# Kernel tuning notes

Hardware: AMD Instinct MI355X
Metric: run time of the kernel (lower is better)

## Reference

```python
import jax, jax.numpy as jnp
import numpy as np

B, T, N, D, M, H, L, FF = 8, 128, 24, 128, 9, 8, 4, 1024
F = D // H          # spatial head dim = 16
HD = D // H         # temporal head dim = 16
ND = N * D          # 3072
NM = N * M          # 216


def setup_inputs() -> dict:
    key = jax.random.key(0)
    ks = jax.random.split(key, 24)
    w = lambda k, shape, s=0.05: (jax.random.normal(k, shape, jnp.float32) * s)
    z = lambda shape: jnp.zeros(shape, jnp.float32)
    return {
        "inputs": jax.random.normal(ks[0], (B, T, NM), jnp.float32),
        "emb_W": w(ks[1], (N, M, D)), "emb_b": z((N, D)),
        "sp_Wq": w(ks[2], (L, H, N, D, F)), "sp_bq": z((L, H, N, F)),
        "sp_Wk": w(ks[3], (L, H, D, F)), "sp_bk": z((L, H, F)),
        "sp_Wv": w(ks[4], (L, H, D, F)), "sp_bv": z((L, H, F)),
        "tmp_Win": w(ks[5], (L, N, 3 * D, D)), "tmp_bin": z((L, N, 3 * D)),
        "tmp_Wout": w(ks[6], (L, N, D, D)), "tmp_bout": z((L, N, D)),
        "ff_W1": w(ks[7], (L, ND, FF)), "ff_b1": z((L, FF)),
        "ff_W2": w(ks[8], (L, FF, ND)), "ff_b2": z((L, ND)),
        "ln_g": jnp.ones((L, ND), jnp.float32), "ln_b": z((L, ND)),
        "fin_W": w(ks[9], (ND, NM)), "fin_b": z((NM,)),
    }


def _ln(x, g, b):
    m = jnp.mean(x, -1, keepdims=True)
    v = jnp.mean(jnp.square(x - m), -1, keepdims=True)
    return (x - m) * jax.lax.rsqrt(v + 1e-5) * g + b


def _pos_encoding():
    # standard sinusoidal PE; original adds it over the FIRST axis of the
    # (B, T, N*D) tensor (applied before the permute), so index by B.
    pos = jnp.arange(B, dtype=jnp.float32)[:, None]
    div = jnp.exp(jnp.arange(0, ND, 2, dtype=jnp.float32) * (-np.log(10000.0) / ND))
    pe = jnp.zeros((B, ND), jnp.float32)
    pe = pe.at[:, 0::2].set(jnp.sin(pos * div)).at[:, 1::2].set(jnp.cos(pos * div))
    return pe


def reference(inputs, emb_W, emb_b, sp_Wq, sp_bq, sp_Wk, sp_bk, sp_Wv, sp_bv,
              tmp_Win, tmp_bin, tmp_Wout, tmp_bout, ff_W1, ff_b1, ff_W2, ff_b2,
              ln_g, ln_b, fin_W, fin_b):
    # joint embedding: (B,T,N,M) @ (N,M,D) -> (B,T,N,D)
    x4 = inputs.reshape(B, T, N, M)
    emb = (jnp.einsum('btnm,nmd->btnd', x4, emb_W) + emb_b).reshape(B, T, ND)
    emb = emb + _pos_encoding()[:, None, :]
    h = emb.transpose(1, 0, 2)                     # (T, B, ND)
    # PyTorch float attn_mask is ADDED to scores: +1.0 strictly below diagonal
    mask = jnp.tril(jnp.ones((T, T), jnp.float32), -1)
    for l in range(L):
        xr = h.reshape(T, B, N, D)
        # ---- spatial attention (shared K/V, per-joint Q, per head) ----
        k = jnp.einsum('tbnd,hdf->tbhnf', xr, sp_Wk[l]) + sp_bk[l][:, None, :]
        v = jnp.einsum('tbnd,hdf->tbhnf', xr, sp_Wv[l]) + sp_bv[l][:, None, :]
        q = jnp.einsum('tbnd,hndf->tbhnf', xr, sp_Wq[l]) + sp_bq[l]
        a = jax.nn.softmax(jnp.einsum('tbhnf,tbhmf->tbhnm', q, k) / jnp.sqrt(jnp.float32(F)), -1)
        sp = jnp.einsum('tbhnm,tbhmf->tbhnf', a, v)
        sp = sp.transpose(0, 1, 3, 2, 4).reshape(T, B, ND)   # joint-major, heads concat within joint
        sp = _ln(sp + h, ln_g[l], ln_b[l])
        # ---- temporal attention (per-joint nn.MultiheadAttention) ----
        Wq_t, Wk_t, Wv_t = tmp_Win[l, :, :D], tmp_Win[l, :, D:2 * D], tmp_Win[l, :, 2 * D:]
        bq_t, bk_t, bv_t = tmp_bin[l, :, :D], tmp_bin[l, :, D:2 * D], tmp_bin[l, :, 2 * D:]
        qt = (jnp.einsum('tbnd,ned->tbne', xr, Wq_t) + bq_t).reshape(T, B, N, H, HD)
        kt = (jnp.einsum('tbnd,ned->tbne', xr, Wk_t) + bk_t).reshape(T, B, N, H, HD)
        vt = (jnp.einsum('tbnd,ned->tbne', xr, Wv_t) + bv_t).reshape(T, B, N, H, HD)
        st = jnp.einsum('tbnhe,sbnhe->bnhts', qt, kt) / jnp.sqrt(jnp.float32(HD)) + mask
        at = jax.nn.softmax(st, -1)
        ot = jnp.einsum('bnhts,sbnhe->tbnhe', at, vt).reshape(T, B, N, D)
        tp = (jnp.einsum('tbnd,nod->tbno', ot, tmp_Wout[l]) + tmp_bout[l]).reshape(T, B, ND)
        tp = _ln(tp + h, ln_g[l], ln_b[l])
        # ---- FFN (no activation in original) + residual + shared LN ----
        a2 = sp + tp
        o = (a2 @ ff_W1[l] + ff_b1[l]) @ ff_W2[l] + ff_b2[l]
        h = _ln(o + a2, ln_g[l], ln_b[l])
    out = h @ fin_W + fin_b                        # (T, B, NM)
    return out.transpose(1, 0, 2) + inputs
```

## Files before the change

### kernel.cpp

```cpp
#include <hip/hip_runtime.h>
#include <hip/hip_bf16.h>
#include <math.h>

constexpr int kB = 8, kT = 128, kN = 24, kD = 128, kM = 9, kH = 8, kL = 4, kFF = 1024;
constexpr int kF = 16;
constexpr int kHD = 16;
constexpr int kND = kN * kD;
constexpr int kNM = kN * kM;
constexpr int kP = kB * kT;

using bf16x8 = __attribute__((ext_vector_type(8))) short;
using f32x4  = __attribute__((ext_vector_type(4))) float;
typedef __hip_bfloat16 bf16;

__device__ __forceinline__ void load_lds16(const void* g, void* l) {
  __builtin_amdgcn_global_load_lds(
      (const __attribute__((address_space(1))) void*)g,
      (__attribute__((address_space(3))) void*)l, 16, 0, 0);
}

template<int BM, int BN, bool OUTBF>
__global__ __launch_bounds__(256) void mfma_gemm(
    const bf16* __restrict__ A, const bf16* __restrict__ Bm,
    const float* __restrict__ bias, void* __restrict__ Cv,
    int M, int Nc, int K, int ldB, int sAi, int sCi,
    long offAg, long offBg, long offCg, int sBg)
{
  constexpr int WM = BM / 2, WN = BN / 2;
  constexpr int MT = WM / 16, NT = WN / 16;
  constexpr int ASLOTS = BM * 4;
  constexpr int BSLOTS = BN * 4;
  __shared__ __align__(16) bf16 As[BM * 32];
  __shared__ __align__(16) bf16 Bs[BN * 32];

  int g = blockIdx.z;
  A  += offAg * g;
  Bm += offBg * g;
  long cbase = offCg * (long)g;
  int bOff = sBg * g;

  int m0 = blockIdx.y * BM, n0 = blockIdx.x * BN;
  int tid = threadIdx.x, lane = tid & 63, wave = tid >> 6;
  int wm = wave >> 1, wn = wave & 1;
  int fr = lane & 15, fq = lane >> 4;

  f32x4 acc[MT][NT] = {};

  for (int kk = 0; kk < K; kk += 32) {
#pragma unroll
    for (int s = tid; s < ASLOTS; s += 256) {
      int m = s >> 2, k8 = (s & 3) * 8;
      load_lds16(A + (size_t)(m0 + m) * sAi + (kk + k8), &As[s * 8]);
    }
#pragma unroll
    for (int s = tid; s < BSLOTS; s += 256) {
      int n = s >> 2, k8 = (s & 3) * 8;
      int nr = n0 + n; if (nr > Nc - 1) nr = Nc - 1;
      load_lds16(Bm + (size_t)nr * ldB + (kk + k8), &Bs[s * 8]);
    }
    __syncthreads();
    bf16x8 af[MT], bf[NT];
#pragma unroll
    for (int i = 0; i < MT; i++)
      af[i] = *(const bf16x8*)&As[(wm * WM + i * 16 + fr) * 32 + fq * 8];
#pragma unroll
    for (int j = 0; j < NT; j++)
      bf[j] = *(const bf16x8*)&Bs[(wn * WN + j * 16 + fr) * 32 + fq * 8];
#pragma unroll
    for (int i = 0; i < MT; i++)
#pragma unroll
      for (int j = 0; j < NT; j++)
        acc[i][j] = __builtin_amdgcn_mfma_f32_16x16x32_bf16(af[i], bf[j], acc[i][j], 0, 0, 0);
    __syncthreads();
  }

#pragma unroll
  for (int i = 0; i < MT; i++) {
    int row = m0 + wm * WM + i * 16 + fq * 4;
#pragma unroll
    for (int j = 0; j < NT; j++) {
      int col = n0 + wn * WN + j * 16 + fr;
      if (col < Nc) {
        float bv = bias ? bias[bOff + col] : 0.f;
#pragma unroll
        for (int r = 0; r < 4; r++) {
          long ci = cbase + (size_t)(row + r) * sCi + col;
          float v = acc[i][j][r] + bv;
          if (OUTBF) ((bf16*)Cv)[ci] = __float2bfloat16(v);
          else       ((float*)Cv)[ci] = v;
        }
      }
    }
  }
}


__global__ __launch_bounds__(256) void trans_cvt_kernel(
    const float* __restrict__ in, bf16* __restrict__ out,
    int R, int C, long inStrideZ, long outStrideZ)
{
  __shared__ float t[64][65];
  int c0 = blockIdx.x * 64, r0 = blockIdx.y * 64;
  in  += inStrideZ  * blockIdx.z;
  out += outStrideZ * blockIdx.z;
  int tx = threadIdx.x & 63, ty = threadIdx.x >> 6;
  for (int rr = ty; rr < 64; rr += 4) {
    int r = r0 + rr, c = c0 + tx;
    t[rr][tx] = (r < R && c < C) ? in[(size_t)r * C + c] : 0.f;
  }
  __syncthreads();
  for (int cc = ty; cc < 64; cc += 4) {
    int c = c0 + cc, r = r0 + tx;
    if (c < C && r < R) out[(size_t)c * R + r] = __float2bfloat16(t[tx][cc]);
  }
}

__global__ __launch_bounds__(256) void cvt_kernel(
    const float* __restrict__ in, bf16* __restrict__ out, int n)
{
  int i = blockIdx.x * 256 + threadIdx.x;
  if (i < n) out[i] = __float2bfloat16(in[i]);
}

__global__ __launch_bounds__(256) void build_spW_kernel(
    const float* __restrict__ Wq, const float* __restrict__ Wk,
    const float* __restrict__ Wv, const float* __restrict__ Win,
    bf16* __restrict__ outW)
{
  int i = blockIdx.x * 256 + threadIdx.x;
  int d = i & 127;
  int rest = i >> 7;
  int r = rest % 768;
  int n = (rest / 768) % 24;
  int l = rest / (768 * 24);
  int hh = (r & 127) >> 4, f = r & 15;
  float v;
  if (r < 128)      v = Wq[((((size_t)l * kH + hh) * kN + n) * kD + d) * kF + f];
  else if (r < 256) v = Wk[(((size_t)l * kH + hh) * kD + d) * kF + f];
  else if (r < 384) v = Wv[(((size_t)l * kH + hh) * kD + d) * kF + f];
  else              v = Win[(((size_t)l * kN + n) * 384 + (r - 384)) * kD + d];
  outW[i] = __float2bfloat16(v);
}

__global__ __launch_bounds__(256) void build_spb_kernel(
    const float* __restrict__ bq, const float* __restrict__ bk,
    const float* __restrict__ bv, const float* __restrict__ bin,
    float* __restrict__ outb)
{
  int i = blockIdx.x * 256 + threadIdx.x;
  if (i >= kL * 24 * 768) return;
  int r = i % 768;
  int n = (i / 768) % 24;
  int l = i / (768 * 24);
  int hh = (r & 127) >> 4, f = r & 15;
  float v;
  if (r < 128)      v = bq[(((size_t)l * kH + hh) * kN + n) * kF + f];
  else if (r < 256) v = bk[((size_t)l * kH + hh) * kF + f];
  else if (r < 384) v = bv[((size_t)l * kH + hh) * kF + f];
  else              v = bin[((size_t)l * kN + n) * 384 + (r - 384)];
  outb[i] = v;
}

__global__ __launch_bounds__(256) void emb_kernel(
    const float* __restrict__ inp, const float* __restrict__ W,
    const float* __restrict__ bias, float* __restrict__ h, bf16* __restrict__ hbb)
{
  int p = blockIdx.x;
  int t = p / kB, b = p % kB;
  __shared__ float xs[kNM];
  for (int i = threadIdx.x; i < kNM; i += 256)
    xs[i] = inp[((size_t)b * kT + t) * kNM + i];
  __syncthreads();
  const float c1 = -logf(10000.f) / (float)kND;
  for (int c = threadIdx.x; c < kND; c += 256) {
    int n = c / kD, d = c % kD;
    float acc = bias[n * kD + d];
#pragma unroll
    for (int m = 0; m < kM; m++)
      acc += xs[n * kM + m] * W[(n * kM + m) * kD + d];
    float ang = (float)b * expf((float)(c & ~1) * c1);
    acc += (c & 1) ? cosf(ang) : sinf(ang);
    h[(size_t)p * kND + c] = acc;
    hbb[(size_t)p * kND + c] = __float2bfloat16(acc);
  }
}

__global__ __launch_bounds__(192) void sp_attn_kernel(
    const bf16* __restrict__ qkv, float* __restrict__ out)
{
  int p = blockIdx.x;
  __shared__ float s[24 * 385];
  for (int i = threadIdx.x; i < 24 * 384; i += 192) {
    int n = i / 384, c = i % 384;
    s[n * 385 + c] = __bfloat162float(qkv[((size_t)n * kP + p) * 768 + c]);
  }
  __syncthreads();
  int hh = threadIdx.x / 24, n = threadIdx.x % 24;
  const float* qr = s + n * 385 + hh * 16;
  float sc[24];
  float mx = -1e30f;
#pragma unroll
  for (int m = 0; m < 24; m++) {
    const float* kr = s + m * 385 + 128 + hh * 16;
    float d = 0.f;
#pragma unroll
    for (int f = 0; f < 16; f++) d += qr[f] * kr[f];
    d *= 0.25f;
    sc[m] = d;
    mx = fmaxf(mx, d);
  }
  float sum = 0.f;
#pragma unroll
  for (int m = 0; m < 24; m++) { float e = __expf(sc[m] - mx); sc[m] = e; sum += e; }
  float inv = 1.f / sum;
  float* orow = out + (size_t)p * kND + n * kD + hh * 16;
#pragma unroll
  for (int f = 0; f < 16; f++) {
    float acc = 0.f;
#pragma unroll
    for (int m = 0; m < 24; m++) acc += sc[m] * s[m * 385 + 256 + hh * 16 + f];
    orow[f] = acc * inv;
  }
}

__global__ __launch_bounds__(128) void t_attn_mfma(
    const bf16* __restrict__ qkv, bf16* __restrict__ ot)
{
  int g = blockIdx.x;
  int hh = g & 7, n = (g >> 3) % 24, b = g / 192;
  __shared__ __align__(16) ushort Qs[128][32];
  __shared__ __align__(16) ushort Ks[128][32];
  __shared__ __align__(16) ushort Vt[16][136];
  __shared__ __align__(16) ushort Ps[128][136];

  for (int idx = threadIdx.x; idx < 1024; idx += 128) {
    int t = idx >> 3, e2 = (idx & 7) * 2;
    const ushort* src = (const ushort*)qkv +
        ((size_t)n * kP + (size_t)t * kB + b) * 768 + 384 + hh * 16 + e2;
    ushort2 q2 = *(const ushort2*)(src);
    ushort2 k2 = *(const ushort2*)(src + 128);
    ushort2 v2 = *(const ushort2*)(src + 256);
    *(ushort2*)&Qs[t][e2] = q2;
    *(ushort2*)&Ks[t][e2] = k2;
    *(ushort2*)&Qs[t][16 + e2] = make_ushort2(0, 0);
    *(ushort2*)&Ks[t][16 + e2] = make_ushort2(0, 0);
    Vt[e2][t] = v2.x;
    Vt[e2 + 1][t] = v2.y;
  }
  __syncthreads();

  int lane = threadIdx.x & 63, w = threadIdx.x >> 6;
  int c = lane & 15, quad = lane >> 4;

  bf16x8 aq[4];
#pragma unroll
  for (int mt = 0; mt < 4; mt++)
    aq[mt] = *(const bf16x8*)&Qs[w * 64 + mt * 16 + c][quad * 8];
  f32x4 acc[4][8];
#pragma unroll
  for (int nt = 0; nt < 8; nt++) {
    bf16x8 bk = *(const bf16x8*)&Ks[nt * 16 + c][quad * 8];
#pragma unroll
    for (int mt = 0; mt < 4; mt++) {
      f32x4 z = {0.f, 0.f, 0.f, 0.f};
      acc[mt][nt] = __builtin_amdgcn_mfma_f32_16x16x32_bf16(aq[mt], bk, z, 0, 0, 0);
    }
  }

  f32x4 invv[4];
#pragma unroll
  for (int mt = 0; mt < 4; mt++) {
    int tbase = w * 64 + mt * 16 + quad * 4;
    f32x4 rm = {-1e30f, -1e30f, -1e30f, -1e30f};
#pragma unroll
    for (int nt = 0; nt < 8; nt++) {
      int s = nt * 16 + c;
#pragma unroll
      for (int r = 0; r < 4; r++) {
        float x = acc[mt][nt][r] * 0.25f + ((s < tbase + r) ? 1.f : 0.f);
        acc[mt][nt][r] = x;
        rm[r] = fmaxf(rm[r], x);
      }
    }
#pragma unroll
    for (int off = 1; off < 16; off <<= 1)
#pragma unroll
      for (int r = 0; r < 4; r++) rm[r] = fmaxf(rm[r], __shfl_xor(rm[r], off, 64));
    f32x4 rs = {0.f, 0.f, 0.f, 0.f};
#pragma unroll
    for (int nt = 0; nt < 8; nt++)
#pragma unroll
      for (int r = 0; r < 4; r++) {
        float pp = __expf(acc[mt][nt][r] - rm[r]);
        acc[mt][nt][r] = pp;
        rs[r] += pp;
      }
#pragma unroll
    for (int off = 1; off < 16; off <<= 1)
#pragma unroll
      for (int r = 0; r < 4; r++) rs[r] += __shfl_xor(rs[r], off, 64);
#pragma unroll
    for (int r = 0; r < 4; r++) invv[mt][r] = 1.f / rs[r];
#pragma unroll
    for (int nt = 0; nt < 8; nt++)
#pragma unroll
      for (int r = 0; r < 4; r++) {
        bf16 pb = __float2bfloat16(acc[mt][nt][r]);
        Ps[tbase + r][nt * 16 + c] = *(ushort*)&pb;
      }
  }

  f32x4 o[4] = {};
#pragma unroll
  for (int ks = 0; ks < 128; ks += 32) {
    bf16x8 bv = *(const bf16x8*)&Vt[c][ks + quad * 8];
#pragma unroll
    for (int mt = 0; mt < 4; mt++) {
      bf16x8 ap = *(const bf16x8*)&Ps[w * 64 + mt * 16 + c][ks + quad * 8];
      o[mt] = __builtin_amdgcn_mfma_f32_16x16x32_bf16(ap, bv, o[mt], 0, 0, 0);
    }
  }

#pragma unroll
  for (int mt = 0; mt < 4; mt++) {
#pragma unroll
    for (int r = 0; r < 4; r++) {
      int t = w * 64 + mt * 16 + quad * 4 + r;
      float val = o[mt][r] * invv[mt][r];
      ot[((size_t)n * kP + (size_t)t * kB + b) * 128 + hh * 16 + c] = __float2bfloat16(val);
    }
  }
}

__global__ __launch_bounds__(256) void fuse_a2_kernel(
    const float* __restrict__ sp, const float* __restrict__ tp,
    const float* __restrict__ h, const float* __restrict__ g,
    const float* __restrict__ be, float* __restrict__ a2, bf16* __restrict__ a2b)
{
  int row = blockIdx.x;
  const float* s1p = sp + (size_t)row * kND;
  const float* s2p = tp + (size_t)row * kND;
  const float* hp  = h  + (size_t)row * kND;
  float x1[12], x2[12];
  float sum1 = 0.f, sum2 = 0.f;
#pragma unroll
  for (int i = 0; i < 12; i++) {
    int c = threadIdx.x + 256 * i;
    float hv = hp[c];
    x1[i] = s1p[c] + hv; x2[i] = s2p[c] + hv;
    sum1 += x1[i]; sum2 += x2[i];
  }
  __shared__ float red1[4], red2[4];
#pragma unroll
  for (int o = 32; o > 0; o >>= 1) { sum1 += __shfl_down(sum1, o, 64); sum2 += __shfl_down(sum2, o, 64); }
  int wid = threadIdx.x >> 6;
  if ((threadIdx.x & 63) == 0) { red1[wid] = sum1; red2[wid] = sum2; }
  __syncthreads();
  float mean1 = (red1[0] + red1[1] + red1[2] + red1[3]) * (1.f / kND);
  float mean2 = (red2[0] + red2[1] + red2[2] + red2[3]) * (1.f / kND);
  __syncthreads();
  float v1 = 0.f, v2 = 0.f;
#pragma unroll
  for (int i = 0; i < 12; i++) {
    float d1 = x1[i] - mean1, d2 = x2[i] - mean2;
    v1 += d1 * d1; v2 += d2 * d2;
  }
#pragma unroll
  for (int o = 32; o > 0; o >>= 1) { v1 += __shfl_down(v1, o, 64); v2 += __shfl_down(v2, o, 64); }
  if ((threadIdx.x & 63) == 0) { red1[wid] = v1; red2[wid] = v2; }
  __syncthreads();
  float r1 = rsqrtf((red1[0] + red1[1] + red1[2] + red1[3]) * (1.f / kND) + 1e-5f);
  float r2 = rsqrtf((red2[0] + red2[1] + red2[2] + red2[3]) * (1.f / kND) + 1e-5f);
#pragma unroll
  for (int i = 0; i < 12; i++) {
    int c = threadIdx.x + 256 * i;
    float gc = g[c], bc = be[c];
    float o = (x1[i] - mean1) * r1 * gc + bc + (x2[i] - mean2) * r2 * gc + bc;
    a2[(size_t)row * kND + c] = o;
    a2b[(size_t)row * kND + c] = __float2bfloat16(o);
  }
}

__global__ __launch_bounds__(256) void add_ln_dual_kernel(
    const float* __restrict__ a, const float* __restrict__ b,
    const float* __restrict__ g, const float* __restrict__ be,
    float* __restrict__ out, bf16* __restrict__ outb)
{
  int row = blockIdx.x;
  const float* ar = a + (size_t)row * kND;
  const float* br = b + (size_t)row * kND;
  float v[12];
  float s = 0.f;
#pragma unroll
  for (int i = 0; i < 12; i++) {
    int c = threadIdx.x + 256 * i;
    float x = ar[c] + br[c];
    v[i] = x; s += x;
  }
  __shared__ float red[4];
#pragma unroll
  for (int o = 32; o > 0; o >>= 1) s += __shfl_down(s, o, 64);
  int wid = threadIdx.x >> 6;
  if ((threadIdx.x & 63) == 0) red[wid] = s;
  __syncthreads();
  float mean = (red[0] + red[1] + red[2] + red[3]) * (1.f / kND);
  __syncthreads();
  float vs = 0.f;
#pragma unroll
  for (int i = 0; i < 12; i++) { float d = v[i] - mean; vs += d * d; }
#pragma unroll
  for (int o = 32; o > 0; o >>= 1) vs += __shfl_down(vs, o, 64);
  if ((threadIdx.x & 63) == 0) red[wid] = vs;
  __syncthreads();
  float rstd = rsqrtf((red[0] + red[1] + red[2] + red[3]) * (1.f / kND) + 1e-5f);
#pragma unroll
  for (int i = 0; i < 12; i++) {
    int c = threadIdx.x + 256 * i;
    float o = (v[i] - mean) * rstd * g[c] + be[c];
    out[(size_t)row * kND + c] = o;
    outb[(size_t)row * kND + c] = __float2bfloat16(o);
  }
}

__global__ __launch_bounds__(256) void ff1_reduce_kernel(
    const float* __restrict__ part, const float* __restrict__ bias,
    bf16* __restrict__ out)
{
  int i4 = (blockIdx.x * 256 + threadIdx.x) * 4;
  const size_t S = (size_t)kP * kFF;
  float4 p0 = *(const float4*)(part + i4);
  float4 p1 = *(const float4*)(part + S + i4);
  float4 p2 = *(const float4*)(part + 2 * S + i4);
  int col = i4 & (kFF - 1);
#pragma unroll
  for (int j = 0; j < 4; j++) {
    float v = ((const float*)&p0)[j] + ((const float*)&p1)[j] + ((const float*)&p2)[j]
            + bias[col + j];
    out[i4 + j] = __float2bfloat16(v);
  }
}

__global__ __launch_bounds__(256) void final_reduce_add_kernel(
    const float* __restrict__ part, const float* __restrict__ fin_b,
    const float* __restrict__ inp, float* __restrict__ out)
{
  int i = blockIdx.x * 256 + threadIdx.x;
  if (i >= kB * kT * kNM) return;
  int c = i % kNM;
  int rem = i / kNM;
  int t = rem % kT, b = rem / kT;
  size_t pi = (size_t)(t * kB + b) * kNM + c;
  const size_t S = (size_t)kP * kNM;
  float v = fin_b[c] + inp[i];
#pragma unroll
  for (int z = 0; z < 8; z++) v += part[z * S + pi];
  out[i] = v;
}

extern "C" void kernel_launch(void* const* d_in, const int* in_sizes, int n_in,
                              void* d_out, int out_size, void* d_ws, size_t ws_size,
                              hipStream_t stream)
{
  const float* inputs   = (const float*)d_in[0];
  const float* emb_W    = (const float*)d_in[1];
  const float* emb_b    = (const float*)d_in[2];
  const float* sp_Wq    = (const float*)d_in[3];
  const float* sp_bq    = (const float*)d_in[4];
  const float* sp_Wk    = (const float*)d_in[5];
  const float* sp_bk    = (const float*)d_in[6];
  const float* sp_Wv    = (const float*)d_in[7];
  const float* sp_bv    = (const float*)d_in[8];
  const float* tmp_Win  = (const float*)d_in[9];
  const float* tmp_bin  = (const float*)d_in[10];
  const float* tmp_Wout = (const float*)d_in[11];
  const float* tmp_bout = (const float*)d_in[12];
  const float* ff_W1    = (const float*)d_in[13];
  const float* ff_b1    = (const float*)d_in[14];
  const float* ff_W2    = (const float*)d_in[15];
  const float* ff_b2    = (const float*)d_in[16];
  const float* ln_g     = (const float*)d_in[17];
  const float* ln_b     = (const float*)d_in[18];
  const float* fin_W    = (const float*)d_in[19];
  const float* fin_b    = (const float*)d_in[20];
  float* out = (float*)d_out;

  char* wp = (char*)d_ws;
  size_t off = 0;
  auto alloc = [&](size_t bytes) { void* p = wp + off; off += (bytes + 255) & ~(size_t)255; return p; };
  bf16* spW   = (bf16*)alloc((size_t)kL * 24 * 768 * 128 * 2);
  bf16* toWb  = (bf16*)alloc((size_t)kL * 24 * 128 * 128 * 2);
  bf16* W1t   = (bf16*)alloc((size_t)kL * kFF * kND * 2);
  bf16* W2t   = (bf16*)alloc((size_t)kL * kND * kFF * 2);
  bf16* finWt = (bf16*)alloc((size_t)kNM * kND * 2);
  float* spbc = (float*)alloc((size_t)kL * 24 * 768 * 4);
  float* hb   = (float*)alloc((size_t)kP * kND * 4);
  bf16*  hbb  = (bf16*) alloc((size_t)kP * kND * 2);
  bf16*  qkvb = (bf16*) alloc((size_t)24 * kP * 768 * 2);
  float* sp   = (float*)alloc((size_t)kP * kND * 4);
  float* tp   = (float*)alloc((size_t)kP * kND * 4);
  float* a2   = (float*)alloc((size_t)kP * kND * 4);
  bf16*  a2b  = (bf16*) alloc((size_t)kP * kND * 2);
  bf16*  f1b  = (bf16*) alloc((size_t)kP * kFF * 2);
  bf16*  otb  = (bf16*) alloc((size_t)24 * kP * 128 * 2);
  float* ffpart  = sp;
  float* finpart = tp;

  trans_cvt_kernel<<<dim3(kFF / 64, kND / 64, kL), 256, 0, stream>>>(
      ff_W1, W1t, kND, kFF, (long)kND * kFF, (long)kFF * kND);
  trans_cvt_kernel<<<dim3(kND / 64, kFF / 64, kL), 256, 0, stream>>>(
      ff_W2, W2t, kFF, kND, (long)kFF * kND, (long)kND * kFF);
  trans_cvt_kernel<<<dim3((kNM + 63) / 64, kND / 64, 1), 256, 0, stream>>>(
      fin_W, finWt, kND, kNM, 0L, 0L);
  cvt_kernel<<<(kL * 24 * 128 * 128 + 255) / 256, 256, 0, stream>>>(
      tmp_Wout, toWb, kL * 24 * 128 * 128);
  build_spW_kernel<<<(kL * 24 * 768 * 128) / 256, 256, 0, stream>>>(
      sp_Wq, sp_Wk, sp_Wv, tmp_Win, spW);
  build_spb_kernel<<<(kL * 24 * 768 + 255) / 256, 256, 0, stream>>>(
      sp_bq, sp_bk, sp_bv, tmp_bin, spbc);

  emb_kernel<<<kP, 256, 0, stream>>>(inputs, emb_W, emb_b, hb, hbb);

  for (int l = 0; l < kL; l++) {
    const float* lg = ln_g + (size_t)l * kND;
    const float* lb = ln_b + (size_t)l * kND;

    mfma_gemm<128, 128, true><<<dim3(6, 8, 24), 256, 0, stream>>>(
        hbb, spW + (size_t)l * 24 * 768 * 128, spbc + (size_t)l * 24 * 768, qkvb,
        kP, 768, 128, 128, kND, 768,
        128, 768 * 128, (long)kP * 768, 768);

    sp_attn_kernel<<<kP, 192, 0, stream>>>(qkvb, sp);
    t_attn_mfma<<<kB * 24 * 8, 128, 0, stream>>>(qkvb, otb);

    mfma_gemm<64, 64, false><<<dim3(2, 16, 24), 256, 0, stream>>>(
        otb, toWb + (size_t)l * 24 * 128 * 128, tmp_bout + (size_t)l * 24 * 128, tp,
        kP, 128, 128, 128, 128, kND,
        (long)kP * 128, 128 * 128, 128, 128);

    fuse_a2_kernel<<<kP, 256, 0, stream>>>(sp, tp, hb, lg, lb, a2, a2b);

    mfma_gemm<64, 64, false><<<dim3(kFF / 64, kP / 64, 3), 256, 0, stream>>>(
        a2b, W1t + (size_t)l * kFF * kND, nullptr, ffpart,
        kP, kFF, kND / 3, kND, kND, kFF,
        kND / 3, kND / 3, (long)kP * kFF, 0);
    ff1_reduce_kernel<<<(kP * kFF / 4) / 256, 256, 0, stream>>>(
        ffpart, ff_b1 + (size_t)l * kFF, f1b);

    mfma_gemm<64, 64, false><<<dim3(kND / 64, kP / 64, 1), 256, 0, stream>>>(
        f1b, W2t + (size_t)l * kND * kFF, ff_b2 + (size_t)l * kND, tp,
        kP, kND, kFF, kFF, kFF, kND, 0, 0, 0, 0);

    add_ln_dual_kernel<<<kP, 256, 0, stream>>>(tp, a2, lg, lb, hb, hbb);
  }

  mfma_gemm<64, 64, false><<<dim3((kNM + 63) / 64, kP / 64, 8), 256, 0, stream>>>(
      hbb, finWt, nullptr, finpart,
      kP, kNM, kND / 8, kND, kND, kNM,
      kND / 8, kND / 8, (long)kP * kNM, 0);
  final_reduce_add_kernel<<<(kB * kT * kNM + 255) / 256, 256, 0, stream>>>(
      finpart, fin_b, inputs, out);
}
```

Baseline: 903.0 us.

## Deepen GEMM K-tile to 64, stage epilogue through LDS, widen attention loads

The MFMA GEMM now loads 64-wide K slices per iteration, which halves the number of barrier pairs per K sweep. Its epilogue stages accumulators through shared memory so each thread writes 16 contiguous outputs with vector stores instead of scattered scalar stores. The spatial and temporal attention kernels load qkv with 4-element vector reads instead of scalar or 2-element reads, and the spatial LDS row stride is padded for float4 alignment. The trade-offs are doubled LDS per block, extra barriers in the epilogue, and an assumption that N is a multiple of 16 columns per chunk.

```diff
diff --git a/kernel.cpp b/kernel.cpp
--- a/kernel.cpp
+++ b/kernel.cpp
@@ -28,10 +28,13 @@
 {
   constexpr int WM = BM / 2, WN = BN / 2;
   constexpr int MT = WM / 16, NT = WN / 16;
-  constexpr int ASLOTS = BM * 4;
-  constexpr int BSLOTS = BN * 4;
-  __shared__ __align__(16) bf16 As[BM * 32];
-  __shared__ __align__(16) bf16 Bs[BN * 32];
+  constexpr int ASLOTS = BM * 8;
+  constexpr int BSLOTS = BN * 8;
+  constexpr int CSTR = BN + 4;
+  __shared__ __align__(16) char smem[(BM + BN) * 64 * 2];
+  bf16* As = (bf16*)smem;
+  bf16* Bs = (bf16*)(smem + BM * 64 * 2);
+  float* Cs = (float*)smem;
 
   int g = blockIdx.z;
   A  += offAg * g;
@@ -46,49 +49,80 @@
 
   f32x4 acc[MT][NT] = {};
 
-  for (int kk = 0; kk < K; kk += 32) {
+  for (int kk = 0; kk < K; kk += 64) {
 #pragma unroll
     for (int s = tid; s < ASLOTS; s += 256) {
-      int m = s >> 2, k8 = (s & 3) * 8;
+      int m = s >> 3, k8 = (s & 7) * 8;
       load_lds16(A + (size_t)(m0 + m) * sAi + (kk + k8), &As[s * 8]);
     }
 #pragma unroll
     for (int s = tid; s < BSLOTS; s += 256) {
-      int n = s >> 2, k8 = (s & 3) * 8;
+      int n = s >> 3, k8 = (s & 7) * 8;
       int nr = n0 + n; if (nr > Nc - 1) nr = Nc - 1;
       load_lds16(Bm + (size_t)nr * ldB + (kk + k8), &Bs[s * 8]);
     }
     __syncthreads();
-    bf16x8 af[MT], bf[NT];
-#pragma unroll
-    for (int i = 0; i < MT; i++)
-      af[i] = *(const bf16x8*)&As[(wm * WM + i * 16 + fr) * 32 + fq * 8];
+#pragma unroll
+    for (int ks = 0; ks < 2; ks++) {
+      bf16x8 af[MT], bfr[NT];
+#pragma unroll
+      for (int i = 0; i < MT; i++)
+        af[i] = *(const bf16x8*)&As[(wm * WM + i * 16 + fr) * 64 + ks * 32 + fq * 8];
+#pragma unroll
+      for (int j = 0; j < NT; j++)
+        bfr[j] = *(const bf16x8*)&Bs[(wn * WN + j * 16 + fr) * 64 + ks * 32 + fq * 8];
+#pragma unroll
+      for (int i = 0; i < MT; i++)
+#pragma unroll
+        for (int j = 0; j < NT; j++)
+          acc[i][j] = __builtin_amdgcn_mfma_f32_16x16x32_bf16(af[i], bfr[j], acc[i][j], 0, 0, 0);
+    }
+    __syncthreads();
+  }
+
+  constexpr int NCHUNK = BN / 16;
+  int tcol = tid & (NCHUNK - 1);
+  int trow = tid / NCHUNK;
+  int colbase = n0 + tcol * 16;
+  float vb[16];
+  if (trow < 32) {
+#pragma unroll
+    for (int jj = 0; jj < 16; jj++)
+      vb[jj] = bias ? bias[bOff + colbase + jj] : 0.f;
+  }
+#pragma unroll
+  for (int i = 0; i < MT; i++) {
+    __syncthreads();
 #pragma unroll
     for (int j = 0; j < NT; j++)
-      bf[j] = *(const bf16x8*)&Bs[(wn * WN + j * 16 + fr) * 32 + fq * 8];
-#pragma unroll
-    for (int i = 0; i < MT; i++)
-#pragma unroll
-      for (int j = 0; j < NT; j++)
-        acc[i][j] = __builtin_amdgcn_mfma_f32_16x16x32_bf16(af[i], bf[j], acc[i][j], 0, 0, 0);
+#pragma unroll
+      for (int r = 0; r < 4; r++)
+        Cs[(wm * 16 + fq * 4 + r) * CSTR + wn * WN + j * 16 + fr] = acc[i][j][r];
     __syncthreads();
-  }
-
-#pragma unroll
-  for (int i = 0; i < MT; i++) {
-    int row = m0 + wm * WM + i * 16 + fq * 4;
-#pragma unroll
-    for (int j = 0; j < NT; j++) {
-      int col = n0 + wn * WN + j * 16 + fr;
-      if (col < Nc) {
-        float bv = bias ? bias[bOff + col] : 0.f;
-#pragma unroll
-        for (int r = 0; r < 4; r++) {
-          long ci = cbase + (size_t)(row + r) * sCi + col;
-          float v = acc[i][j][r] + bv;
-          if (OUTBF) ((bf16*)Cv)[ci] = __float2bfloat16(v);
-          else       ((float*)Cv)[ci] = v;
+    if (trow < 32) {
+      int row = m0 + (trow >> 4) * WM + i * 16 + (trow & 15);
+      float vals[16];
+#pragma unroll
+      for (int jj = 0; jj < 4; jj++)
+        *(float4*)&vals[jj * 4] = *(const float4*)&Cs[trow * CSTR + tcol * 16 + jj * 4];
+#pragma unroll
+      for (int jj = 0; jj < 16; jj++) vals[jj] += vb[jj];
+      if (OUTBF) {
+        bf16* cp = (bf16*)Cv + cbase + (size_t)row * sCi + colbase;
+        union { bf16 h[8]; uint4 v; } pk;
+#pragma unroll
+        for (int half = 0; half < 2; half++) {
+          if (colbase + half * 8 + 8 <= Nc) {
+#pragma unroll
+            for (int jj = 0; jj < 8; jj++) pk.h[jj] = __float2bfloat16(vals[half * 8 + jj]);
+            *(uint4*)(cp + half * 8) = pk.v;
+          }
         }
+      } else {
+        float* cp = (float*)Cv + cbase + (size_t)row * sCi + colbase;
+#pragma unroll
+        for (int jj = 0; jj < 4; jj++)
+          if (colbase + jj * 4 + 4 <= Nc) *(float4*)(cp + jj * 4) = *(float4*)&vals[jj * 4];
       }
     }
   }
@@ -189,19 +223,25 @@
     const bf16* __restrict__ qkv, float* __restrict__ out)
 {
   int p = blockIdx.x;
-  __shared__ float s[24 * 385];
-  for (int i = threadIdx.x; i < 24 * 384; i += 192) {
-    int n = i / 384, c = i % 384;
-    s[n * 385 + c] = __bfloat162float(qkv[((size_t)n * kP + p) * 768 + c]);
+  __shared__ float s[24 * 388];
+  for (int i = threadIdx.x; i < 2304; i += 192) {
+    int n = i / 96, c4 = (i % 96) * 4;
+    ushort4 u = *(const ushort4*)((const ushort*)qkv + ((size_t)n * kP + p) * 768 + c4);
+    float4 f;
+    f.x = __bfloat162float(*(const bf16*)&u.x);
+    f.y = __bfloat162float(*(const bf16*)&u.y);
+    f.z = __bfloat162float(*(const bf16*)&u.z);
+    f.w = __bfloat162float(*(const bf16*)&u.w);
+    *(float4*)&s[n * 388 + c4] = f;
   }
   __syncthreads();
   int hh = threadIdx.x / 24, n = threadIdx.x % 24;
-  const float* qr = s + n * 385 + hh * 16;
+  const float* qr = s + n * 388 + hh * 16;
   float sc[24];
   float mx = -1e30f;
 #pragma unroll
   for (int m = 0; m < 24; m++) {
-    const float* kr = s + m * 385 + 128 + hh * 16;
+    const float* kr = s + m * 388 + 128 + hh * 16;
     float d = 0.f;
 #pragma unroll
     for (int f = 0; f < 16; f++) d += qr[f] * kr[f];
@@ -218,7 +258,7 @@
   for (int f = 0; f < 16; f++) {
     float acc = 0.f;
 #pragma unroll
-    for (int m = 0; m < 24; m++) acc += sc[m] * s[m * 385 + 256 + hh * 16 + f];
+    for (int m = 0; m < 24; m++) acc += sc[m] * s[m * 388 + 256 + hh * 16 + f];
     orow[f] = acc * inv;
   }
 }
@@ -233,19 +273,18 @@
   __shared__ __align__(16) ushort Vt[16][136];
   __shared__ __align__(16) ushort Ps[128][136];
 
-  for (int idx = threadIdx.x; idx < 1024; idx += 128) {
-    int t = idx >> 3, e2 = (idx & 7) * 2;
+  for (int idx = threadIdx.x; idx < 512; idx += 128) {
+    int t = idx >> 2, e4 = (idx & 3) * 4;
     const ushort* src = (const ushort*)qkv +
-        ((size_t)n * kP + (size_t)t * kB + b) * 768 + 384 + hh * 16 + e2;
-    ushort2 q2 = *(const ushort2*)(src);
-    ushort2 k2 = *(const ushort2*)(src + 128);
-    ushort2 v2 = *(const ushort2*)(src + 256);
-    *(ushort2*)&Qs[t][e2] = q2;
-    *(ushort2*)&Ks[t][e2] = k2;
-    *(ushort2*)&Qs[t][16 + e2] = make_ushort2(0, 0);
-    *(ushort2*)&Ks[t][16 + e2] = make_ushort2(0, 0);
-    Vt[e2][t] = v2.x;
-    Vt[e2 + 1][t] = v2.y;
+        ((size_t)n * kP + (size_t)t * kB + b) * 768 + 384 + hh * 16 + e4;
+    ushort4 q4 = *(const ushort4*)(src);
+    ushort4 k4 = *(const ushort4*)(src + 128);
+    ushort4 v4 = *(const ushort4*)(src + 256);
+    *(ushort4*)&Qs[t][e4] = q4;
+    *(ushort4*)&Ks[t][e4] = k4;
+    *(ushort4*)&Qs[t][16 + e4] = make_ushort4(0, 0, 0, 0);
+    *(ushort4*)&Ks[t][16 + e4] = make_ushort4(0, 0, 0, 0);
+    Vt[e4][t] = v4.x; Vt[e4 + 1][t] = v4.y; Vt[e4 + 2][t] = v4.z; Vt[e4 + 3][t] = v4.w;
   }
   __syncthreads();
 
```

After: 897.1 us. About the same (-0.7%).
